# Performance work log

Measured on AMD Instinct MI355X. Metric: run time of the kernel, lower is better.

The kernel has to match this reference:

```python
import jax, jax.numpy as jnp
import numpy as np

N = 100000   # nodes
E = 640000   # edges (before self-loops)
G = 1000     # graphs in batch
D_IN = 100
D = 128
EPS = 1e-5


def setup_inputs() -> dict:
    key = jax.random.key(0)
    ks = jax.random.split(key, 12)
    x = jax.random.normal(ks[0], (N, D_IN), dtype=jnp.float32)
    edge_index = jax.random.randint(ks[1], (2, E), 0, N, dtype=jnp.int64)
    edge_weight = jax.random.uniform(ks[2], (E,), dtype=jnp.float32)
    batch = jnp.sort(jax.random.randint(ks[3], (N,), 0, G, dtype=jnp.int64))
    def glorot(k, shape):
        fan = shape[0]
        return jax.random.normal(k, shape, dtype=jnp.float32) / np.float32(np.sqrt(fan))
    return {
        "x": x, "edge_index": edge_index, "edge_weight": edge_weight, "batch": batch,
        "W0": glorot(ks[4], (D_IN, D)), "b0": jnp.zeros((D,), jnp.float32),
        "W1": glorot(ks[5], (D, D)),    "b1": jnp.zeros((D,), jnp.float32),
        "W2": glorot(ks[6], (D, D)),    "b2": jnp.zeros((D,), jnp.float32),
        "gamma": jnp.ones((3, D), jnp.float32), "beta": jnp.zeros((3, D), jnp.float32),
        "run_mean": jnp.zeros((3, D), jnp.float32), "run_var": jnp.ones((3, D), jnp.float32),
        "Wout": glorot(ks[7], (D, 1)), "bout": jnp.zeros((1,), jnp.float32),
    }


def reference(x, edge_index, edge_weight, batch, W0, b0, W1, b1, W2, b2,
              gamma, beta, run_mean, run_var, Wout, bout):
    n = x.shape[0]
    # add self-loops with weight 1 (GCNConv default)
    loop = jnp.arange(n, dtype=edge_index.dtype)
    src = jnp.concatenate([edge_index[0], loop])
    dst = jnp.concatenate([edge_index[1], loop])
    ew = jnp.concatenate([edge_weight, jnp.ones((n,), edge_weight.dtype)])
    # symmetric normalization: D^{-1/2} A D^{-1/2}
    deg = jax.ops.segment_sum(ew, dst, num_segments=n)
    dinv = jnp.where(deg > 0, jax.lax.rsqrt(deg), 0.0)
    norm = dinv[src] * ew * dinv[dst]            # [E+N]

    def gcn_bn_relu(h, W, b, g, bt, rm, rv):
        h = h @ W                                 # linear first (cheaper gather dim)
        agg = jax.ops.segment_sum(h[src] * norm[:, None], dst, num_segments=n)
        agg = agg + b
        # BatchNorm1d in eval mode (running stats); dropout is identity in eval
        agg = g * (agg - rm) * jax.lax.rsqrt(rv + EPS) + bt
        return jax.nn.relu(agg)

    h = gcn_bn_relu(x, W0, b0, gamma[0], beta[0], run_mean[0], run_var[0])
    h = gcn_bn_relu(h, W1, b1, gamma[1], beta[1], run_mean[1], run_var[1])
    h = gcn_bn_relu(h, W2, b2, gamma[2], beta[2], run_mean[2], run_var[2])

    # global mean pool over graphs
    counts = jax.ops.segment_sum(jnp.ones((n,), h.dtype), batch, num_segments=G)
    pooled = jax.ops.segment_sum(h, batch, num_segments=G) / jnp.maximum(counts, 1.0)[:, None]
    return pooled @ Wout + bout
```

## Files before the change

### kernel.cpp

```cpp
#include <hip/hip_runtime.h>

#define BN_EPS 1e-5f
#define BINCAP 32

static inline size_t align_up(size_t x, size_t a) { return (x + a - 1) & ~(a - 1); }

typedef __attribute__((ext_vector_type(8))) short bf16x8;
typedef __attribute__((ext_vector_type(4))) float f32x4;

__device__ __forceinline__ void bf16split(float v, unsigned short& hi, unsigned short& lo) {
    unsigned u = __float_as_uint(v);
    unsigned rh = (u + 0x7FFFu + ((u >> 16) & 1u)) >> 16;
    float fh = __uint_as_float(rh << 16);
    hi = (unsigned short)rh;
    float rem = v - fh;
    unsigned u2 = __float_as_uint(rem);
    lo = (unsigned short)((u2 + 0x7FFFu + ((u2 >> 16) & 1u)) >> 16);
}

__device__ __forceinline__ unsigned short bf16rne(float v) {
    unsigned u = __float_as_uint(v);
    return (unsigned short)((u + 0x7FFFu + ((u >> 16) & 1u)) >> 16);
}

__device__ __forceinline__ float chlo(unsigned u) { return __uint_as_float(u << 16); }
__device__ __forceinline__ float chhi(unsigned u) { return __uint_as_float(u & 0xffff0000u); }



__global__ void place_kernel(const int* __restrict__ src, const int* __restrict__ dst,
                             const float* __restrict__ ew,
                             int* __restrict__ cntc, int2* __restrict__ bins, int E) {
    int e = blockIdx.x * blockDim.x + threadIdx.x;
    if (e >= E) return;
    int d = dst[e];
    int pos = atomicAdd(&cntc[d], 1);
    if (pos < BINCAP)
        bins[(size_t)d * BINCAP + pos] = make_int2(src[e], __float_as_int(ew[e]));
}


__global__ void deginv_kernel(const int* __restrict__ cntc, const int2* __restrict__ bins,
                              float* __restrict__ dinv, int N) {
    int i = blockIdx.x * blockDim.x + threadIdx.x;
    if (i >= N) return;
    int cnt = cntc[i]; if (cnt > BINCAP) cnt = BINCAP;
    const int2* b = bins + (size_t)i * BINCAP;
    float s = 0.f;
    for (int j = 0; j < cnt; ++j) s += __int_as_float(b[j].y);
    dinv[i] = rsqrtf(s + 1.0f);
}


__global__ void normfix_kernel(const int* __restrict__ cntc, int2* __restrict__ bins,
                               const float* __restrict__ dinv, int N) {
    int i = blockIdx.x * blockDim.x + threadIdx.x;
    if (i >= N) return;
    int cnt = cntc[i]; if (cnt > BINCAP) cnt = BINCAP;
    float di = dinv[i];
    int2* b = bins + (size_t)i * BINCAP;
    for (int j = 0; j < cnt; ++j) {
        int2 pr = b[j];
        float w = __int_as_float(pr.y) * dinv[pr.x] * di;
        b[j].y = __float_as_int(w);
    }
}


__global__ void prep_kernel(const float* __restrict__ W0, const float* __restrict__ W1,
                            const float* __restrict__ W2, int K0,
                            unsigned short* __restrict__ Whi, unsigned short* __restrict__ Wlo,
                            const float* __restrict__ gamma, const float* __restrict__ beta,
                            const float* __restrict__ rm, const float* __restrict__ rv,
                            const float* __restrict__ b0, const float* __restrict__ b1,
                            const float* __restrict__ b2,
                            float* __restrict__ scale, float* __restrict__ shift,
                            const int* __restrict__ batch, int* __restrict__ gstart,
                            int N, int G) {
    int idx = blockIdx.x * blockDim.x + threadIdx.x;
    if (idx < 3 * 32 * 64 * 8) {
        int j    = idx & 7;
        int lane = (idx >> 3) & 63;
        int f    = (idx >> 9) & 31;
        int l    = idx >> 14;
        int ct = f >> 2, k0c = f & 3;
        int quad = lane >> 4, m16 = lane & 15;
        int n = ct * 16 + m16;
        int k = k0c * 32 + quad * 8 + j;
        const float* W = (l == 0) ? W0 : (l == 1) ? W1 : W2;
        int Kl = (l == 0) ? K0 : 128;
        float v = (k < Kl) ? W[(size_t)k * 128 + n] : 0.f;
        unsigned short hi, lo;
        bf16split(v, hi, lo);
        Whi[idx] = hi;
        Wlo[idx] = lo;
    } else if (idx < 3 * 32 * 64 * 8 + 384) {
        int t = idx - 3 * 32 * 64 * 8;
        int l = t >> 7, j = t & 127;
        const float* bs = (l == 0) ? b0 : (l == 1) ? b1 : b2;
        float sc = gamma[t] * rsqrtf(rv[t] + BN_EPS);
        scale[t] = sc;
        shift[t] = beta[t] + (bs[j] - rm[t]) * sc;
    } else {
        int i = idx - (3 * 32 * 64 * 8 + 384);
        if (i >= N) return;
        int b = batch[i];
        int prev = (i == 0) ? -1 : batch[i - 1];
        for (int g = prev + 1; g <= b; ++g) gstart[g] = i;
        if (i == N - 1) {
            for (int g = b + 1; g <= G; ++g) gstart[g] = N;
        }
    }
}


__device__ __forceinline__ void mfma_tail(const bf16x8 ah[4], const bf16x8 al[4],
                                          const unsigned short* __restrict__ Whi,
                                          const unsigned short* __restrict__ Wlo,
                                          unsigned short* __restrict__ Yh,
                                          int row0, int quad, int m16, int lane, int N) {
    const bf16x8* Wh8 = (const bf16x8*)Whi;
    const bf16x8* Wl8 = (const bf16x8*)Wlo;

    f32x4 acc[8];
    #pragma unroll
    for (int ct = 0; ct < 8; ++ct) acc[ct] = (f32x4){0.f, 0.f, 0.f, 0.f};

    bf16x8 bh[2][4], bl[2][4];
    #pragma unroll
    for (int k0c = 0; k0c < 4; ++k0c) {
        bh[0][k0c] = Wh8[k0c * 64 + lane];
        bl[0][k0c] = Wl8[k0c * 64 + lane];
    }

    __builtin_amdgcn_s_setprio(1);
    #pragma unroll
    for (int ct = 0; ct < 8; ++ct) {
        int cur = ct & 1, nxt = cur ^ 1;
        if (ct < 7) {
            #pragma unroll
            for (int k0c = 0; k0c < 4; ++k0c) {
                bh[nxt][k0c] = Wh8[((ct + 1) * 4 + k0c) * 64 + lane];
                bl[nxt][k0c] = Wl8[((ct + 1) * 4 + k0c) * 64 + lane];
            }
        }
        #pragma unroll
        for (int k0c = 0; k0c < 4; ++k0c) {
            acc[ct] = __builtin_amdgcn_mfma_f32_16x16x32_bf16(ah[k0c], bh[cur][k0c], acc[ct], 0, 0, 0);
            acc[ct] = __builtin_amdgcn_mfma_f32_16x16x32_bf16(ah[k0c], bl[cur][k0c], acc[ct], 0, 0, 0);
            acc[ct] = __builtin_amdgcn_mfma_f32_16x16x32_bf16(al[k0c], bh[cur][k0c], acc[ct], 0, 0, 0);
        }
    }
    __builtin_amdgcn_s_setprio(0);

    #pragma unroll
    for (int ct = 0; ct < 8; ++ct) {
        #pragma unroll
        for (int rg = 0; rg < 4; ++rg) {
            int row = row0 + quad * 4 + rg;
            if (row < N)
                Yh[(size_t)row * 128 + ct * 16 + m16] = bf16rne(acc[ct][rg]);
        }
    }
}


__launch_bounds__(256, 2)
__global__ void gemm0_fused_kernel(const float* __restrict__ x, int D_IN,
                                   const unsigned short* __restrict__ Whi,
                                   const unsigned short* __restrict__ Wlo,
                                   unsigned short* __restrict__ Yh, int N) {
    int tid = threadIdx.x;
    int wid = tid >> 6, lane = tid & 63;
    int quad = lane >> 4, m16 = lane & 15;
    int row0 = blockIdx.x * 64 + wid * 16;

    int arow = row0 + m16;
    if (arow > N - 1) arow = N - 1;
    const float* xr = x + (size_t)arow * D_IN;

    bf16x8 ah[4], al[4];
    #pragma unroll
    for (int k0c = 0; k0c < 4; ++k0c) {
        int kb = k0c * 32 + quad * 8;
        float vs[8];
        if (kb + 8 <= D_IN) {
            float4 v0 = *((const float4*)(xr + kb));
            float4 v1 = *((const float4*)(xr + kb + 4));
            vs[0] = v0.x; vs[1] = v0.y; vs[2] = v0.z; vs[3] = v0.w;
            vs[4] = v1.x; vs[5] = v1.y; vs[6] = v1.z; vs[7] = v1.w;
        } else {
            #pragma unroll
            for (int j = 0; j < 8; ++j) vs[j] = (kb + j < D_IN) ? xr[kb + j] : 0.f;
        }
        #pragma unroll
        for (int j = 0; j < 8; ++j) {
            unsigned short hi, lo;
            bf16split(vs[j], hi, lo);
            ah[k0c][j] = (short)hi;
            al[k0c][j] = (short)lo;
        }
    }

    mfma_tail(ah, al, Whi, Wlo, Yh, row0, quad, m16, lane, N);
}


__device__ __forceinline__ void gather_pair(const unsigned* __restrict__ Yh32,
                                            int2 pr0, int m0, int2 pr1, int m1,
                                            int lane,
                                            float& ax0, float& ay0, float& ax1, float& ay1) {
    int mr0 = (m0 + 7) & ~7, mr1 = (m1 + 7) & ~7;
    int mr = mr0 > mr1 ? mr0 : mr1;
    for (int j = 0; j < mr; j += 8) {
        int a0 = __builtin_amdgcn_readlane(pr0.x, j);
        int a1 = __builtin_amdgcn_readlane(pr0.x, j + 1);
        int a2 = __builtin_amdgcn_readlane(pr0.x, j + 2);
        int a3 = __builtin_amdgcn_readlane(pr0.x, j + 3);
        int a4 = __builtin_amdgcn_readlane(pr0.x, j + 4);
        int a5 = __builtin_amdgcn_readlane(pr0.x, j + 5);
        int a6 = __builtin_amdgcn_readlane(pr0.x, j + 6);
        int a7 = __builtin_amdgcn_readlane(pr0.x, j + 7);
        int b0 = __builtin_amdgcn_readlane(pr1.x, j);
        int b1 = __builtin_amdgcn_readlane(pr1.x, j + 1);
        int b2 = __builtin_amdgcn_readlane(pr1.x, j + 2);
        int b3 = __builtin_amdgcn_readlane(pr1.x, j + 3);
        int b4 = __builtin_amdgcn_readlane(pr1.x, j + 4);
        int b5 = __builtin_amdgcn_readlane(pr1.x, j + 5);
        int b6 = __builtin_amdgcn_readlane(pr1.x, j + 6);
        int b7 = __builtin_amdgcn_readlane(pr1.x, j + 7);
        float wa0 = __int_as_float(__builtin_amdgcn_readlane(pr0.y, j));
        float wa1 = __int_as_float(__builtin_amdgcn_readlane(pr0.y, j + 1));
        float wa2 = __int_as_float(__builtin_amdgcn_readlane(pr0.y, j + 2));
        float wa3 = __int_as_float(__builtin_amdgcn_readlane(pr0.y, j + 3));
        float wa4 = __int_as_float(__builtin_amdgcn_readlane(pr0.y, j + 4));
        float wa5 = __int_as_float(__builtin_amdgcn_readlane(pr0.y, j + 5));
        float wa6 = __int_as_float(__builtin_amdgcn_readlane(pr0.y, j + 6));
        float wa7 = __int_as_float(__builtin_amdgcn_readlane(pr0.y, j + 7));
        float wb0 = __int_as_float(__builtin_amdgcn_readlane(pr1.y, j));
        float wb1 = __int_as_float(__builtin_amdgcn_readlane(pr1.y, j + 1));
        float wb2 = __int_as_float(__builtin_amdgcn_readlane(pr1.y, j + 2));
        float wb3 = __int_as_float(__builtin_amdgcn_readlane(pr1.y, j + 3));
        float wb4 = __int_as_float(__builtin_amdgcn_readlane(pr1.y, j + 4));
        float wb5 = __int_as_float(__builtin_amdgcn_readlane(pr1.y, j + 5));
        float wb6 = __int_as_float(__builtin_amdgcn_readlane(pr1.y, j + 6));
        float wb7 = __int_as_float(__builtin_amdgcn_readlane(pr1.y, j + 7));
        unsigned ua0 = Yh32[(size_t)a0 * 64 + lane];
        unsigned ua1 = Yh32[(size_t)a1 * 64 + lane];
        unsigned ua2 = Yh32[(size_t)a2 * 64 + lane];
        unsigned ua3 = Yh32[(size_t)a3 * 64 + lane];
        unsigned ua4 = Yh32[(size_t)a4 * 64 + lane];
        unsigned ua5 = Yh32[(size_t)a5 * 64 + lane];
        unsigned ua6 = Yh32[(size_t)a6 * 64 + lane];
        unsigned ua7 = Yh32[(size_t)a7 * 64 + lane];
        unsigned ub0 = Yh32[(size_t)b0 * 64 + lane];
        unsigned ub1 = Yh32[(size_t)b1 * 64 + lane];
        unsigned ub2 = Yh32[(size_t)b2 * 64 + lane];
        unsigned ub3 = Yh32[(size_t)b3 * 64 + lane];
        unsigned ub4 = Yh32[(size_t)b4 * 64 + lane];
        unsigned ub5 = Yh32[(size_t)b5 * 64 + lane];
        unsigned ub6 = Yh32[(size_t)b6 * 64 + lane];
        unsigned ub7 = Yh32[(size_t)b7 * 64 + lane];
        ax0 += chlo(ua0) * wa0; ay0 += chhi(ua0) * wa0;
        ax0 += chlo(ua1) * wa1; ay0 += chhi(ua1) * wa1;
        ax0 += chlo(ua2) * wa2; ay0 += chhi(ua2) * wa2;
        ax0 += chlo(ua3) * wa3; ay0 += chhi(ua3) * wa3;
        ax0 += chlo(ua4) * wa4; ay0 += chhi(ua4) * wa4;
        ax0 += chlo(ua5) * wa5; ay0 += chhi(ua5) * wa5;
        ax0 += chlo(ua6) * wa6; ay0 += chhi(ua6) * wa6;
        ax0 += chlo(ua7) * wa7; ay0 += chhi(ua7) * wa7;
        ax1 += chlo(ub0) * wb0; ay1 += chhi(ub0) * wb0;
        ax1 += chlo(ub1) * wb1; ay1 += chhi(ub1) * wb1;
        ax1 += chlo(ub2) * wb2; ay1 += chhi(ub2) * wb2;
        ax1 += chlo(ub3) * wb3; ay1 += chhi(ub3) * wb3;
        ax1 += chlo(ub4) * wb4; ay1 += chhi(ub4) * wb4;
        ax1 += chlo(ub5) * wb5; ay1 += chhi(ub5) * wb5;
        ax1 += chlo(ub6) * wb6; ay1 += chhi(ub6) * wb6;
        ax1 += chlo(ub7) * wb7; ay1 += chhi(ub7) * wb7;
    }
}


__launch_bounds__(64, 4)
__global__ void fused_agg_gemm_kernel(
        const unsigned* __restrict__ Yh_in,
        const int2* __restrict__ bins, const int* __restrict__ cntc,
        const float* __restrict__ dinv,
        const float* __restrict__ scale, const float* __restrict__ shift,
        const unsigned short* __restrict__ Whi, const unsigned short* __restrict__ Wlo,
        unsigned short* __restrict__ Yh_out, int N) {
    __shared__ float sA[16 * 132];
    int lane = threadIdx.x;
    int quad = lane >> 4, m16 = lane & 15;
    int row0 = blockIdx.x * 16;

    float2 sc = ((const float2*)scale)[lane];
    float2 sh = ((const float2*)shift)[lane];

    int mm[16]; float dv[16]; unsigned uh[16]; int2 gg[16];
    #pragma unroll
    for (int i = 0; i < 16; ++i) {
        int n = row0 + i; if (n > N - 1) n = N - 1;
        mm[i] = cntc[n];
        dv[i] = dinv[n];
        uh[i] = Yh_in[(size_t)n * 64 + lane];
    }
    #pragma unroll
    for (int i = 0; i < 16; ++i) {
        int n = row0 + i; if (n > N - 1) n = N - 1;
        int m = mm[i]; if (m > BINCAP) m = BINCAP;
        mm[i] = m;
        gg[i] = (lane < m) ? bins[(size_t)n * BINCAP + lane] : make_int2(n, 0);
    }

    #pragma unroll
    for (int i = 0; i < 16; i += 2) {
        float w00 = dv[i] * dv[i], w01 = dv[i + 1] * dv[i + 1];
        float ax0 = chlo(uh[i]) * w00,     ay0 = chhi(uh[i]) * w00;
        float ax1 = chlo(uh[i + 1]) * w01, ay1 = chhi(uh[i + 1]) * w01;
        gather_pair(Yh_in, gg[i], mm[i], gg[i + 1], mm[i + 1], lane, ax0, ay0, ax1, ay1);
        float ox0 = fmaxf(ax0 * sc.x + sh.x, 0.f);
        float oy0 = fmaxf(ay0 * sc.y + sh.y, 0.f);
        float ox1 = fmaxf(ax1 * sc.x + sh.x, 0.f);
        float oy1 = fmaxf(ay1 * sc.y + sh.y, 0.f);
        *((float2*)&sA[i * 132 + 2 * lane])       = make_float2(ox0, oy0);
        *((float2*)&sA[(i + 1) * 132 + 2 * lane]) = make_float2(ox1, oy1);
    }

    asm volatile("s_waitcnt lgkmcnt(0)" ::: "memory");
    __builtin_amdgcn_sched_barrier(0);

    bf16x8 ah[4], al[4];
    #pragma unroll
    for (int k0c = 0; k0c < 4; ++k0c) {
        float4 v0 = *((const float4*)&sA[m16 * 132 + k0c * 32 + quad * 8]);
        float4 v1 = *((const float4*)&sA[m16 * 132 + k0c * 32 + quad * 8 + 4]);
        float vs[8] = {v0.x, v0.y, v0.z, v0.w, v1.x, v1.y, v1.z, v1.w};
        #pragma unroll
        for (int j = 0; j < 8; ++j) {
            unsigned short hi, lo;
            bf16split(vs[j], hi, lo);
            ah[k0c][j] = (short)hi;
            al[k0c][j] = (short)lo;
        }
    }

    mfma_tail(ah, al, Whi, Wlo, Yh_out, row0, quad, m16, lane, N);
}


__launch_bounds__(256)
__global__ void agg3_kernel(const unsigned* __restrict__ Yh32,
                            const int2* __restrict__ bins, const int* __restrict__ cntc,
                            const float* __restrict__ dinv,
                            const float* __restrict__ scale, const float* __restrict__ shift,
                            const float* __restrict__ Wout,
                            float* __restrict__ snode, int N) {
    int idx = blockIdx.x * blockDim.x + threadIdx.x;
    int pairid = idx >> 6, lane = idx & 63;
    int n0 = pairid * 2;
    if (n0 >= N) return;
    int n1 = n0 + 1; if (n1 > N - 1) n1 = n0;

    int m0 = cntc[n0];
    int m1 = cntc[n1];
    float d0 = dinv[n0], d1 = dinv[n1];
    unsigned uh0 = Yh32[(size_t)n0 * 64 + lane];
    unsigned uh1 = Yh32[(size_t)n1 * 64 + lane];
    if (m0 > BINCAP) m0 = BINCAP;
    if (m1 > BINCAP) m1 = BINCAP;
    int2 pr0 = (lane < m0) ? bins[(size_t)n0 * BINCAP + lane] : make_int2(n0, 0);
    int2 pr1 = (lane < m1) ? bins[(size_t)n1 * BINCAP + lane] : make_int2(n1, 0);

    float w00 = d0 * d0, w01 = d1 * d1;
    float ax0 = chlo(uh0) * w00, ay0 = chhi(uh0) * w00;
    float ax1 = chlo(uh1) * w01, ay1 = chhi(uh1) * w01;
    gather_pair(Yh32, pr0, m0, pr1, m1, lane, ax0, ay0, ax1, ay1);

    float2 sc = ((const float2*)scale)[lane];
    float2 sh = ((const float2*)shift)[lane];
    float2 w  = ((const float2*)Wout)[lane];
    float ox0 = fmaxf(ax0 * sc.x + sh.x, 0.f);
    float oy0 = fmaxf(ay0 * sc.y + sh.y, 0.f);
    float ox1 = fmaxf(ax1 * sc.x + sh.x, 0.f);
    float oy1 = fmaxf(ay1 * sc.y + sh.y, 0.f);
    float s0 = ox0 * w.x + oy0 * w.y;
    float s1 = ox1 * w.x + oy1 * w.y;
    #pragma unroll
    for (int off = 32; off > 0; off >>= 1) {
        s0 += __shfl_down(s0, off, 64);
        s1 += __shfl_down(s1, off, 64);
    }
    if (lane == 0) {
        snode[n0] = s0;
        if (n1 != n0) snode[n1] = s1;
    }
}


__launch_bounds__(256)
__global__ void pool3_kernel(const float* __restrict__ snode, const int* __restrict__ gstart,
                             const float* __restrict__ bout, float* __restrict__ out, int G) {
    int g = blockIdx.x;
    int beg = gstart[g], end = gstart[g + 1];
    int t = threadIdx.x;
    float acc = 0.f;
    for (int n = beg + t; n < end; n += 256) acc += snode[n];
    __shared__ float lds[256];
    lds[t] = acc;
    __syncthreads();
    if (t < 64) lds[t] = lds[t] + lds[t + 64] + lds[t + 128] + lds[t + 192];
    __syncthreads();
    if (t < 64) {
        float s = lds[t];
        #pragma unroll
        for (int off = 32; off > 0; off >>= 1) s += __shfl_down(s, off, 64);
        if (t == 0) {
            float cntf = (float)(end - beg);
            out[g] = s / fmaxf(cntf, 1.0f) + bout[0];
        }
    }
}


extern "C" void kernel_launch(void* const* d_in, const int* in_sizes, int n_in,
                              void* d_out, int out_size, void* d_ws, size_t ws_size,
                              hipStream_t stream) {
    const float* x     = (const float*)d_in[0];
    const int*   ei    = (const int*)d_in[1];
    const float* ew    = (const float*)d_in[2];
    const int*   batch = (const int*)d_in[3];
    const float* W0 = (const float*)d_in[4];
    const float* b0 = (const float*)d_in[5];
    const float* W1 = (const float*)d_in[6];
    const float* b1 = (const float*)d_in[7];
    const float* W2 = (const float*)d_in[8];
    const float* b2 = (const float*)d_in[9];
    const float* gamma = (const float*)d_in[10];
    const float* beta  = (const float*)d_in[11];
    const float* rmean = (const float*)d_in[12];
    const float* rvar  = (const float*)d_in[13];
    const float* Wout  = (const float*)d_in[14];
    const float* bout  = (const float*)d_in[15];

    const int E = in_sizes[2];
    const int N = in_sizes[3];
    const int D_IN = in_sizes[0] / N;
    const int G = out_size;

    const int* src = ei;
    const int* dst = ei + E;

    char* ws = (char*)d_ws;
    size_t off = 0;
    float* dinv  = (float*)(ws + off); off = align_up(off + (size_t)N * 4, 256);
    int* cntc    = (int*)(ws + off);   off = align_up(off + (size_t)N * 4, 256);
    int* gstart  = (int*)(ws + off);   off = align_up(off + ((size_t)G + 1) * 4, 256);
    int2* bins   = (int2*)(ws + off);  off = align_up(off + (size_t)N * BINCAP * 8, 256);
    unsigned short* YAh = (unsigned short*)(ws + off); off = align_up(off + (size_t)N * 128 * 2, 256);
    unsigned short* YBh = (unsigned short*)(ws + off); off = align_up(off + (size_t)N * 128 * 2, 256);
    unsigned short* Whi = (unsigned short*)(ws + off); off = align_up(off + 3 * 16384 * 2, 256);
    unsigned short* Wlo = (unsigned short*)(ws + off); off = align_up(off + 3 * 16384 * 2, 256);
    float* scale = (float*)(ws + off); off = align_up(off + 3 * 128 * 4, 256);
    float* shift = (float*)(ws + off); off = align_up(off + 3 * 128 * 4, 256);
    float* snode = (float*)(ws + off); off = align_up(off + (size_t)N * 4, 256);
    (void)ws_size;

    hipMemsetAsync(cntc, 0, (size_t)N * 4, stream);

    const int tB = 256;
    place_kernel<<<(E + tB - 1) / tB, tB, 0, stream>>>(src, dst, ew, cntc, bins, E);
    deginv_kernel<<<(N + tB - 1) / tB, tB, 0, stream>>>(cntc, bins, dinv, N);
    normfix_kernel<<<(N + tB - 1) / tB, tB, 0, stream>>>(cntc, bins, dinv, N);
    {
        int prep_threads = 3 * 32 * 64 * 8 + 384 + N;
        prep_kernel<<<(prep_threads + tB - 1) / tB, tB, 0, stream>>>(
            W0, W1, W2, D_IN, Whi, Wlo,
            gamma, beta, rmean, rvar, b0, b1, b2, scale, shift,
            batch, gstart, N, G);
    }

    int gemm0_blocks = (N + 63) / 64;
    int fused_blocks = (N + 15) / 16;

    gemm0_fused_kernel<<<gemm0_blocks, 256, 0, stream>>>(x, D_IN, Whi, Wlo, YAh, N);
    fused_agg_gemm_kernel<<<fused_blocks, 64, 0, stream>>>(
        (const unsigned*)YAh, bins, cntc, dinv,
        scale, shift, Whi + 16384, Wlo + 16384, YBh, N);
    fused_agg_gemm_kernel<<<fused_blocks, 64, 0, stream>>>(
        (const unsigned*)YBh, bins, cntc, dinv,
        scale + 128, shift + 128, Whi + 2 * 16384, Wlo + 2 * 16384, YAh, N);
    {
        long nthread_pair = (long)((N + 1) / 2) * 64;
        int blocks_pair = (int)((nthread_pair + tB - 1) / tB);
        agg3_kernel<<<blocks_pair, tB, 0, stream>>>((const unsigned*)YAh,
            bins, cntc, dinv, scale + 256, shift + 256, Wout, snode, N);
    }

    pool3_kernel<<<G, 256, 0, stream>>>(snode, gstart, bout, (float*)d_out, G);
}
```

Before: 313.4 us.

## Merge preprocessing and first GEMM into one cooperative kernel with grid syncs

Combines edge placement, weight and BN preparation, degree inverse, the first GEMM and norm fixup into one persistent cooperative kernel separated by grid-wide syncs, replacing five launches. Edge placement now reads four edges per thread with vector loads. The agg3 kernel is relaunched with 64-thread blocks, one block per node pair. It trades launch gaps for a grid-stride loop on a capped grid of 512 blocks, which may lower parallelism for the atomic-heavy placement and GEMM phases, and keeps a multi-kernel fallback if the cooperative launch fails.

```diff
diff --git a/kernel.cpp b/kernel.cpp
--- a/kernel.cpp
+++ b/kernel.cpp
@@ -1,4 +1,7 @@
 #include <hip/hip_runtime.h>
+#include <hip/hip_cooperative_groups.h>
+
+namespace cg = cooperative_groups;
 
 #define BN_EPS 1e-5f
 #define BINCAP 32
@@ -28,87 +31,104 @@
 
 
 
-__global__ void place_kernel(const int* __restrict__ src, const int* __restrict__ dst,
-                             const float* __restrict__ ew,
-                             int* __restrict__ cntc, int2* __restrict__ bins, int E) {
-    int e = blockIdx.x * blockDim.x + threadIdx.x;
-    if (e >= E) return;
-    int d = dst[e];
-    int pos = atomicAdd(&cntc[d], 1);
-    if (pos < BINCAP)
-        bins[(size_t)d * BINCAP + pos] = make_int2(src[e], __float_as_int(ew[e]));
-}
-
-
-__global__ void deginv_kernel(const int* __restrict__ cntc, const int2* __restrict__ bins,
-                              float* __restrict__ dinv, int N) {
-    int i = blockIdx.x * blockDim.x + threadIdx.x;
-    if (i >= N) return;
-    int cnt = cntc[i]; if (cnt > BINCAP) cnt = BINCAP;
-    const int2* b = bins + (size_t)i * BINCAP;
-    float s = 0.f;
-    for (int j = 0; j < cnt; ++j) s += __int_as_float(b[j].y);
-    dinv[i] = rsqrtf(s + 1.0f);
-}
-
-
-__global__ void normfix_kernel(const int* __restrict__ cntc, int2* __restrict__ bins,
-                               const float* __restrict__ dinv, int N) {
-    int i = blockIdx.x * blockDim.x + threadIdx.x;
-    if (i >= N) return;
-    int cnt = cntc[i]; if (cnt > BINCAP) cnt = BINCAP;
-    float di = dinv[i];
-    int2* b = bins + (size_t)i * BINCAP;
-    for (int j = 0; j < cnt; ++j) {
-        int2 pr = b[j];
-        float w = __int_as_float(pr.y) * dinv[pr.x] * di;
-        b[j].y = __float_as_int(w);
-    }
-}
-
-
-__global__ void prep_kernel(const float* __restrict__ W0, const float* __restrict__ W1,
-                            const float* __restrict__ W2, int K0,
-                            unsigned short* __restrict__ Whi, unsigned short* __restrict__ Wlo,
-                            const float* __restrict__ gamma, const float* __restrict__ beta,
-                            const float* __restrict__ rm, const float* __restrict__ rv,
-                            const float* __restrict__ b0, const float* __restrict__ b1,
-                            const float* __restrict__ b2,
-                            float* __restrict__ scale, float* __restrict__ shift,
-                            const int* __restrict__ batch, int* __restrict__ gstart,
-                            int N, int G) {
-    int idx = blockIdx.x * blockDim.x + threadIdx.x;
-    if (idx < 3 * 32 * 64 * 8) {
-        int j    = idx & 7;
-        int lane = (idx >> 3) & 63;
-        int f    = (idx >> 9) & 31;
-        int l    = idx >> 14;
-        int ct = f >> 2, k0c = f & 3;
-        int quad = lane >> 4, m16 = lane & 15;
-        int n = ct * 16 + m16;
-        int k = k0c * 32 + quad * 8 + j;
-        const float* W = (l == 0) ? W0 : (l == 1) ? W1 : W2;
-        int Kl = (l == 0) ? K0 : 128;
-        float v = (k < Kl) ? W[(size_t)k * 128 + n] : 0.f;
-        unsigned short hi, lo;
-        bf16split(v, hi, lo);
-        Whi[idx] = hi;
-        Wlo[idx] = lo;
-    } else if (idx < 3 * 32 * 64 * 8 + 384) {
-        int t = idx - 3 * 32 * 64 * 8;
-        int l = t >> 7, j = t & 127;
-        const float* bs = (l == 0) ? b0 : (l == 1) ? b1 : b2;
-        float sc = gamma[t] * rsqrtf(rv[t] + BN_EPS);
-        scale[t] = sc;
-        shift[t] = beta[t] + (bs[j] - rm[t]) * sc;
-    } else {
-        int i = idx - (3 * 32 * 64 * 8 + 384);
-        if (i >= N) return;
-        int b = batch[i];
-        int prev = (i == 0) ? -1 : batch[i - 1];
-        for (int g = prev + 1; g <= b; ++g) gstart[g] = i;
-        if (i == N - 1) {
-            for (int g = b + 1; g <= G; ++g) gstart[g] = N;
+struct MegaArgs {
+    const int* src; const int* dst; const float* ew;
+    int* cntc; int2* bins; int E;
+    float* dinv; int N;
+    const float* W0; const float* W1; const float* W2; int K0;
+    unsigned short* Whi; unsigned short* Wlo;
+    const float* gamma; const float* beta; const float* rm; const float* rv;
+    const float* b0; const float* b1; const float* b2;
+    float* scale; float* shiftv;
+    const int* batch; int* gstart; int G;
+    const float* x; unsigned short* YAh;
+};
+
+
+__device__ __forceinline__ void place_range(int tid, int nth, const MegaArgs& a) {
+    int nquads = (a.E + 3) >> 2;
+    for (int q = tid; q < nquads; q += nth) {
+        int e0 = q * 4;
+        if (e0 + 4 <= a.E) {
+            int4   s4 = *(const int4*)(a.src + e0);
+            int4   d4 = *(const int4*)(a.dst + e0);
+            float4 w4 = *(const float4*)(a.ew + e0);
+            int p0 = atomicAdd(&a.cntc[d4.x], 1);
+            int p1 = atomicAdd(&a.cntc[d4.y], 1);
+            int p2 = atomicAdd(&a.cntc[d4.z], 1);
+            int p3 = atomicAdd(&a.cntc[d4.w], 1);
+            if (p0 < BINCAP) a.bins[(size_t)d4.x * BINCAP + p0] = make_int2(s4.x, __float_as_int(w4.x));
+            if (p1 < BINCAP) a.bins[(size_t)d4.y * BINCAP + p1] = make_int2(s4.y, __float_as_int(w4.y));
+            if (p2 < BINCAP) a.bins[(size_t)d4.z * BINCAP + p2] = make_int2(s4.z, __float_as_int(w4.z));
+            if (p3 < BINCAP) a.bins[(size_t)d4.w * BINCAP + p3] = make_int2(s4.w, __float_as_int(w4.w));
+        } else {
+            for (int e = e0; e < a.E; ++e) {
+                int d = a.dst[e];
+                int pos = atomicAdd(&a.cntc[d], 1);
+                if (pos < BINCAP)
+                    a.bins[(size_t)d * BINCAP + pos] = make_int2(a.src[e], __float_as_int(a.ew[e]));
+            }
+        }
+    }
+}
+
+__device__ __forceinline__ void prep_range(int tid, int nth, const MegaArgs& a) {
+    int total = 3 * 32 * 64 * 8 + 384 + a.N;
+    for (int idx = tid; idx < total; idx += nth) {
+        if (idx < 3 * 32 * 64 * 8) {
+            int j    = idx & 7;
+            int lane = (idx >> 3) & 63;
+            int f    = (idx >> 9) & 31;
+            int l    = idx >> 14;
+            int ct = f >> 2, k0c = f & 3;
+            int quad = lane >> 4, m16 = lane & 15;
+            int n = ct * 16 + m16;
+            int k = k0c * 32 + quad * 8 + j;
+            const float* W = (l == 0) ? a.W0 : (l == 1) ? a.W1 : a.W2;
+            int Kl = (l == 0) ? a.K0 : 128;
+            float v = (k < Kl) ? W[(size_t)k * 128 + n] : 0.f;
+            unsigned short hi, lo;
+            bf16split(v, hi, lo);
+            a.Whi[idx] = hi;
+            a.Wlo[idx] = lo;
+        } else if (idx < 3 * 32 * 64 * 8 + 384) {
+            int t = idx - 3 * 32 * 64 * 8;
+            int l = t >> 7, j = t & 127;
+            const float* bs = (l == 0) ? a.b0 : (l == 1) ? a.b1 : a.b2;
+            float sc = a.gamma[t] * rsqrtf(a.rv[t] + BN_EPS);
+            a.scale[t] = sc;
+            a.shiftv[t] = a.beta[t] + (bs[j] - a.rm[t]) * sc;
+        } else {
+            int i = idx - (3 * 32 * 64 * 8 + 384);
+            int b = a.batch[i];
+            int prev = (i == 0) ? -1 : a.batch[i - 1];
+            for (int g = prev + 1; g <= b; ++g) a.gstart[g] = i;
+            if (i == a.N - 1) {
+                for (int g = b + 1; g <= a.G; ++g) a.gstart[g] = a.N;
+            }
+        }
+    }
+}
+
+__device__ __forceinline__ void deginv_range(int tid, int nth, const MegaArgs& a) {
+    for (int i = tid; i < a.N; i += nth) {
+        int cnt = a.cntc[i]; if (cnt > BINCAP) cnt = BINCAP;
+        const int2* b = a.bins + (size_t)i * BINCAP;
+        float s = 0.f;
+        for (int j = 0; j < cnt; ++j) s += __int_as_float(b[j].y);
+        a.dinv[i] = rsqrtf(s + 1.0f);
+    }
+}
+
+__device__ __forceinline__ void normfix_range(int tid, int nth, const MegaArgs& a) {
+    for (int i = tid; i < a.N; i += nth) {
+        int cnt = a.cntc[i]; if (cnt > BINCAP) cnt = BINCAP;
+        float di = a.dinv[i];
+        int2* b = a.bins + (size_t)i * BINCAP;
+        for (int j = 0; j < cnt; ++j) {
+            int2 pr = b[j];
+            float w = __int_as_float(pr.y) * a.dinv[pr.x] * di;
+            b[j].y = __float_as_int(w);
         }
     }
 }
@@ -165,19 +185,14 @@
 }
 
 
-__launch_bounds__(256, 2)
-__global__ void gemm0_fused_kernel(const float* __restrict__ x, int D_IN,
-                                   const unsigned short* __restrict__ Whi,
-                                   const unsigned short* __restrict__ Wlo,
-                                   unsigned short* __restrict__ Yh, int N) {
-    int tid = threadIdx.x;
-    int wid = tid >> 6, lane = tid & 63;
-    int quad = lane >> 4, m16 = lane & 15;
-    int row0 = blockIdx.x * 64 + wid * 16;
+__device__ __forceinline__ void gemm0_tile(int tile, const MegaArgs& a,
+                                           int wid, int lane, int quad, int m16) {
+    int row0 = tile * 64 + wid * 16;
+    int N = a.N, D_IN = a.K0;
 
     int arow = row0 + m16;
     if (arow > N - 1) arow = N - 1;
-    const float* xr = x + (size_t)arow * D_IN;
+    const float* xr = a.x + (size_t)arow * D_IN;
 
     bf16x8 ah[4], al[4];
     #pragma unroll
@@ -202,7 +217,55 @@
         }
     }
 
-    mfma_tail(ah, al, Whi, Wlo, Yh, row0, quad, m16, lane, N);
+    mfma_tail(ah, al, a.Whi, a.Wlo, a.YAh, row0, quad, m16, lane, N);
+}
+
+
+__launch_bounds__(256, 2)
+__global__ void mega_kernel(MegaArgs a) {
+    cg::grid_group grid = cg::this_grid();
+    int tid = blockIdx.x * 256 + threadIdx.x;
+    int nth = gridDim.x * 256;
+
+    place_range(tid, nth, a);
+    prep_range(tid, nth, a);
+    __threadfence();
+    grid.sync();
+
+    deginv_range(tid, nth, a);
+    {
+        int wid = threadIdx.x >> 6, lane = threadIdx.x & 63;
+        int quad = lane >> 4, m16 = lane & 15;
+        int ntiles = (a.N + 63) >> 6;
+        for (int t = blockIdx.x; t < ntiles; t += gridDim.x)
+            gemm0_tile(t, a, wid, lane, quad, m16);
+    }
+    __threadfence();
+    grid.sync();
+
+    normfix_range(tid, nth, a);
+}
+
+
+__global__ void place_kernel(MegaArgs a) {
+    place_range(blockIdx.x * blockDim.x + threadIdx.x, gridDim.x * blockDim.x, a);
+}
+__global__ void deginv_kernel(MegaArgs a) {
+    deginv_range(blockIdx.x * blockDim.x + threadIdx.x, gridDim.x * blockDim.x, a);
+}
+__global__ void normfix_kernel(MegaArgs a) {
+    normfix_range(blockIdx.x * blockDim.x + threadIdx.x, gridDim.x * blockDim.x, a);
+}
+__global__ void prep_kernel(MegaArgs a) {
+    prep_range(blockIdx.x * blockDim.x + threadIdx.x, gridDim.x * blockDim.x, a);
+}
+__launch_bounds__(256, 2)
+__global__ void gemm0_kernel(MegaArgs a) {
+    int wid = threadIdx.x >> 6, lane = threadIdx.x & 63;
+    int quad = lane >> 4, m16 = lane & 15;
+    int ntiles = (a.N + 63) >> 6;
+    for (int t = blockIdx.x; t < ntiles; t += gridDim.x)
+        gemm0_tile(t, a, wid, lane, quad, m16);
 }
 
 
@@ -349,15 +412,15 @@
 }
 
 
-__launch_bounds__(256)
+__launch_bounds__(64)
 __global__ void agg3_kernel(const unsigned* __restrict__ Yh32,
                             const int2* __restrict__ bins, const int* __restrict__ cntc,
                             const float* __restrict__ dinv,
                             const float* __restrict__ scale, const float* __restrict__ shift,
                             const float* __restrict__ Wout,
                             float* __restrict__ snode, int N) {
-    int idx = blockIdx.x * blockDim.x + threadIdx.x;
-    int pairid = idx >> 6, lane = idx & 63;
+    int pairid = blockIdx.x;
+    int lane = threadIdx.x;
     int n0 = pairid * 2;
     if (n0 >= N) return;
     int n1 = n0 + 1; if (n1 > N - 1) n1 = n0;
@@ -468,34 +531,54 @@
 
     hipMemsetAsync(cntc, 0, (size_t)N * 4, stream);
 
+    MegaArgs ma;
+    ma.src = src; ma.dst = dst; ma.ew = ew;
+    ma.cntc = cntc; ma.bins = bins; ma.E = E;
+    ma.dinv = dinv; ma.N = N;
+    ma.W0 = W0; ma.W1 = W1; ma.W2 = W2; ma.K0 = D_IN;
+    ma.Whi = Whi; ma.Wlo = Wlo;
+    ma.gamma = gamma; ma.beta = beta; ma.rm = rmean; ma.rv = rvar;
+    ma.b0 = b0; ma.b1 = b1; ma.b2 = b2;
+    ma.scale = scale; ma.shiftv = shift;
+    ma.batch = batch; ma.gstart = gstart; ma.G = G;
+    ma.x = x; ma.YAh = YAh;
+
     const int tB = 256;
-    place_kernel<<<(E + tB - 1) / tB, tB, 0, stream>>>(src, dst, ew, cntc, bins, E);
-    deginv_kernel<<<(N + tB - 1) / tB, tB, 0, stream>>>(cntc, bins, dinv, N);
-    normfix_kernel<<<(N + tB - 1) / tB, tB, 0, stream>>>(cntc, bins, dinv, N);
+
+    bool coop_ok = false;
     {
+        int occ = 0;
+        hipError_t oe = hipOccupancyMaxActiveBlocksPerMultiprocessor(&occ, mega_kernel, 256, 0);
+        int grid = 512;
+        if (oe == hipSuccess && occ >= 1) {
+            int cap = occ * 256;
+            if (cap < grid) grid = cap;
+        }
+        void* kargs[1] = { (void*)&ma };
+        hipError_t ce = hipLaunchCooperativeKernel((const void*)mega_kernel,
+                                                   dim3(grid), dim3(256), kargs, 0, stream);
+        coop_ok = (ce == hipSuccess);
+    }
+    if (!coop_ok) {
+        int nquads = (E + 3) / 4;
+        place_kernel<<<(nquads + tB - 1) / tB, tB, 0, stream>>>(ma);
+        deginv_kernel<<<(N + tB - 1) / tB, tB, 0, stream>>>(ma);
+        normfix_kernel<<<(N + tB - 1) / tB, tB, 0, stream>>>(ma);
         int prep_threads = 3 * 32 * 64 * 8 + 384 + N;
-        prep_kernel<<<(prep_threads + tB - 1) / tB, tB, 0, stream>>>(
-            W0, W1, W2, D_IN, Whi, Wlo,
-            gamma, beta, rmean, rvar, b0, b1, b2, scale, shift,
-            batch, gstart, N, G);
-    }
-
-    int gemm0_blocks = (N + 63) / 64;
+        prep_kernel<<<(prep_threads + tB - 1) / tB, tB, 0, stream>>>(ma);
+        gemm0_kernel<<<(N + 63) / 64, 256, 0, stream>>>(ma);
+    }
+
     int fused_blocks = (N + 15) / 16;
 
-    gemm0_fused_kernel<<<gemm0_blocks, 256, 0, stream>>>(x, D_IN, Whi, Wlo, YAh, N);
     fused_agg_gemm_kernel<<<fused_blocks, 64, 0, stream>>>(
         (const unsigned*)YAh, bins, cntc, dinv,
         scale, shift, Whi + 16384, Wlo + 16384, YBh, N);
     fused_agg_gemm_kernel<<<fused_blocks, 64, 0, stream>>>(
         (const unsigned*)YBh, bins, cntc, dinv,
         scale + 128, shift + 128, Whi + 2 * 16384, Wlo + 2 * 16384, YAh, N);
-    {
-        long nthread_pair = (long)((N + 1) / 2) * 64;
-        int blocks_pair = (int)((nthread_pair + tB - 1) / tB);
-        agg3_kernel<<<blocks_pair, tB, 0, stream>>>((const unsigned*)YAh,
-            bins, cntc, dinv, scale + 256, shift + 256, Wout, snode, N);
-    }
+    agg3_kernel<<<(N + 1) / 2, 64, 0, stream>>>((const unsigned*)YAh,
+        bins, cntc, dinv, scale + 256, shift + 256, Wout, snode, N);
 
     pool3_kernel<<<G, 256, 0, stream>>>(snode, gstart, bout, (float*)d_out, G);
 }
```

After: 499.5 us. +59.4%, slower.
